# Kernel tuning notes

Measured on AMD Instinct MI355X. Metric: run time of the kernel, lower is better.

## Reference

```python
import jax, jax.numpy as jnp
import numpy as np
from jax import lax

K = 3
STRIDE = 1
PAD = 1
DIL = 1


def _rrsvm(x, s):
    # x: [B, C, H, W], s: [C, K, K]
    B, C, H, W = x.shape
    # im2col: [B, C*K*K, Ho, Wo], channel-major patch ordering -> reshape (C, K*K)
    patches = lax.conv_general_dilated_patches(
        x, (K, K), (STRIDE, STRIDE), [(PAD, PAD), (PAD, PAD)],
        rhs_dilation=(DIL, DIL))
    Ho, Wo = patches.shape[2], patches.shape[3]
    p = patches.reshape(B, C, K * K, Ho, Wo)
    # descending sort of each window's values (rank pooling order)
    order = jnp.argsort(-p, axis=2)                      # [B, C, K*K, Ho, Wo]
    sorted_p = jnp.take_along_axis(p, order, axis=2)
    # learned per-rank weights, per channel
    out = jnp.einsum('bckhw,ck->bchw', sorted_p, s.reshape(C, K * K))
    indices = jnp.transpose(order, (0, 1, 3, 4, 2))      # [B, C, Ho, Wo, K*K]
    return out, indices


def setup_inputs() -> dict:
    key = jax.random.key(0)
    k1, k2 = jax.random.split(key)
    B, C, H, W = 16, 128, 56, 56
    x = jax.random.normal(k1, (B, C, H, W), dtype=jnp.float32)
    # module inits s to 1/(C*K*K); use random positive weights for a non-degenerate test
    s = jax.random.uniform(k2, (C, K, K), dtype=jnp.float32) / (K * K)
    return {"x": x, "s": s}


def reference(x, s):
    return _rrsvm(x, s)
```

## Files before the change

### kernel.cpp

```cpp
#include <hip/hip_runtime.h>


#define B_ 16
#define C_ 128
#define H_ 56
#define W_ 56
#define NPIX (B_*C_*H_*W_)
#define BLK 256
#define PXB (BLK * 2)

typedef float v4f __attribute__((ext_vector_type(4)));

__device__ __forceinline__ void sort9(float v[9], float id[9]) {
    #pragma unroll
    for (int rnd = 0; rnd < 9; ++rnd) {
        #pragma unroll
        for (int i = (rnd & 1); i + 1 < 9; i += 2) {
            float vi = v[i], vj = v[i + 1];
            float ii = id[i], ij = id[i + 1];
            bool sw = vj > vi;
            v[i]      = sw ? vj : vi;  v[i + 1]  = sw ? vi : vj;
            id[i]     = sw ? ij : ii;  id[i + 1] = sw ? ii : ij;
        }
    }
}

__global__ __launch_bounds__(BLK) void rrsvm_kernel(
    const float* __restrict__ x, const float* __restrict__ s,
    float* __restrict__ out, float* __restrict__ idxout)
{
    __shared__ float lds[PXB * 9];

    const int tid = threadIdx.x;
    const int pix = (blockIdx.x * BLK + tid) * 2;
    const int w0  = pix % W_;
    const int t   = pix / W_;
    const int h   = t % H_;
    const int bc  = t / H_;
    const int c   = bc & (C_ - 1);

    const float* sp = s + c * 9;
    float sw9[9];
    #pragma unroll
    for (int r = 0; r < 9; ++r) sw9[r] = sp[r];

    const float* img = x + (size_t)bc * (H_ * W_);
    const int r0 = (h > 0)       ? h - 1  : 0;
    const int r2 = (h < H_ - 1)  ? h + 1  : H_ - 1;
    const int c0 = (w0 > 0)      ? w0 - 1 : 0;
    const int c3 = (w0 < W_ - 2) ? w0 + 2 : W_ - 1;
    const float* p0 = img + r0 * W_;
    const float* p1 = img + h  * W_;
    const float* p2 = img + r2 * W_;

    float tap[3][4];
    tap[0][0] = p0[c0]; tap[0][1] = p0[w0]; tap[0][2] = p0[w0 + 1]; tap[0][3] = p0[c3];
    tap[1][0] = p1[c0]; tap[1][1] = p1[w0]; tap[1][2] = p1[w0 + 1]; tap[1][3] = p1[c3];
    tap[2][0] = p2[c0]; tap[2][1] = p2[w0]; tap[2][2] = p2[w0 + 1]; tap[2][3] = p2[c3];

    const bool rv0 = (h > 0), rv2 = (h < H_ - 1);
    const bool cvL = (w0 > 0), cvR = (w0 < W_ - 2);
    tap[0][0] = (rv0 && cvL) ? tap[0][0] : 0.0f;
    tap[0][1] = rv0          ? tap[0][1] : 0.0f;
    tap[0][2] = rv0          ? tap[0][2] : 0.0f;
    tap[0][3] = (rv0 && cvR) ? tap[0][3] : 0.0f;
    tap[1][0] = cvL          ? tap[1][0] : 0.0f;
    tap[1][3] = cvR          ? tap[1][3] : 0.0f;
    tap[2][0] = (rv2 && cvL) ? tap[2][0] : 0.0f;
    tap[2][1] = rv2          ? tap[2][1] : 0.0f;
    tap[2][2] = rv2          ? tap[2][2] : 0.0f;
    tap[2][3] = (rv2 && cvR) ? tap[2][3] : 0.0f;

    float* lbase = lds + tid * 18;
    float2 o;

    {
        float v[9]  = { tap[0][0], tap[0][1], tap[0][2],
                        tap[1][0], tap[1][1], tap[1][2],
                        tap[2][0], tap[2][1], tap[2][2] };
        float id[9] = { 0, 1, 2, 3, 4, 5, 6, 7, 8 };
        sort9(v, id);
        float acc = 0.0f;
        #pragma unroll
        for (int r = 0; r < 9; ++r) acc = fmaf(v[r], sw9[r], acc);
        o.x = acc;
        #pragma unroll
        for (int r = 0; r < 9; ++r) lbase[r] = id[r];
    }
    {
        float v[9]  = { tap[0][1], tap[0][2], tap[0][3],
                        tap[1][1], tap[1][2], tap[1][3],
                        tap[2][1], tap[2][2], tap[2][3] };
        float id[9] = { 0, 1, 2, 3, 4, 5, 6, 7, 8 };
        sort9(v, id);
        float acc = 0.0f;
        #pragma unroll
        for (int r = 0; r < 9; ++r) acc = fmaf(v[r], sw9[r], acc);
        o.y = acc;
        #pragma unroll
        for (int r = 0; r < 9; ++r) lbase[9 + r] = id[r];
    }

    *(float2*)(out + pix) = o;

    __syncthreads();

    v4f* dst = (v4f*)(idxout + (size_t)blockIdx.x * (PXB * 9));
    const v4f* src = (const v4f*)lds;
    __builtin_nontemporal_store(src[tid],        dst + tid);
    __builtin_nontemporal_store(src[tid + 256],  dst + tid + 256);
    __builtin_nontemporal_store(src[tid + 512],  dst + tid + 512);
    __builtin_nontemporal_store(src[tid + 768],  dst + tid + 768);
    if (tid < 128)
        __builtin_nontemporal_store(src[tid + 1024], dst + tid + 1024);
}

extern "C" void kernel_launch(void* const* d_in, const int* in_sizes, int n_in,
                              void* d_out, int out_size, void* d_ws, size_t ws_size,
                              hipStream_t stream) {
    const float* x = (const float*)d_in[0];
    const float* s = (const float*)d_in[1];
    float* out    = (float*)d_out;
    float* idxout = out + NPIX;

    const int nblocks = NPIX / PXB;
    rrsvm_kernel<<<nblocks, BLK, 0, stream>>>(x, s, out, idxout);
}
```

Before: 279.3 us.

## Process four pixels per thread and store indices directly without LDS staging

Each thread now handles four horizontally adjacent pixels, reusing a 3x6 tap window loaded with vector reads. The LDS transpose and block barrier for the index output are removed, and each thread writes its 36 indices with nine 16-byte stores. This cuts redundant loads and the barrier. In exchange it uses more registers, has strided per-instruction stores, and drops the nontemporal hints.

```diff
diff --git a/kernel.cpp b/kernel.cpp
--- a/kernel.cpp
+++ b/kernel.cpp
@@ -7,7 +7,7 @@
 #define W_ 56
 #define NPIX (B_*C_*H_*W_)
 #define BLK 256
-#define PXB (BLK * 2)
+#define PXT 4
 
 typedef float v4f __attribute__((ext_vector_type(4)));
 
@@ -29,15 +29,13 @@
     const float* __restrict__ x, const float* __restrict__ s,
     float* __restrict__ out, float* __restrict__ idxout)
 {
-    __shared__ float lds[PXB * 9];
-
-    const int tid = threadIdx.x;
-    const int pix = (blockIdx.x * BLK + tid) * 2;
-    const int w0  = pix % W_;
-    const int t   = pix / W_;
-    const int h   = t % H_;
-    const int bc  = t / H_;
-    const int c   = bc & (C_ - 1);
+    const int gtid = blockIdx.x * BLK + threadIdx.x;
+    const int pix0 = gtid * PXT;
+    const int w0   = pix0 % W_;
+    const int t    = pix0 / W_;
+    const int h    = t % H_;
+    const int bc   = t / H_;
+    const int c    = bc & (C_ - 1);
 
     const float* sp = s + c * 9;
     float sw9[9];
@@ -45,74 +43,65 @@
     for (int r = 0; r < 9; ++r) sw9[r] = sp[r];
 
     const float* img = x + (size_t)bc * (H_ * W_);
-    const int r0 = (h > 0)       ? h - 1  : 0;
-    const int r2 = (h < H_ - 1)  ? h + 1  : H_ - 1;
-    const int c0 = (w0 > 0)      ? w0 - 1 : 0;
-    const int c3 = (w0 < W_ - 2) ? w0 + 2 : W_ - 1;
+    const int r0 = (h > 0)      ? h - 1 : 0;
+    const int r2 = (h < H_ - 1) ? h + 1 : H_ - 1;
+    const int cl = (w0 > 0)        ? w0 - 1 : 0;
+    const int cr = (w0 < W_ - PXT) ? w0 + 4 : W_ - 1;
     const float* p0 = img + r0 * W_;
     const float* p1 = img + h  * W_;
     const float* p2 = img + r2 * W_;
 
-    float tap[3][4];
-    tap[0][0] = p0[c0]; tap[0][1] = p0[w0]; tap[0][2] = p0[w0 + 1]; tap[0][3] = p0[c3];
-    tap[1][0] = p1[c0]; tap[1][1] = p1[w0]; tap[1][2] = p1[w0 + 1]; tap[1][3] = p1[c3];
-    tap[2][0] = p2[c0]; tap[2][1] = p2[w0]; tap[2][2] = p2[w0 + 1]; tap[2][3] = p2[c3];
+    float T[3][6];
+    {
+        v4f m0 = *(const v4f*)(p0 + w0);
+        v4f m1 = *(const v4f*)(p1 + w0);
+        v4f m2 = *(const v4f*)(p2 + w0);
+        T[0][0] = p0[cl]; T[0][1] = m0.x; T[0][2] = m0.y; T[0][3] = m0.z; T[0][4] = m0.w; T[0][5] = p0[cr];
+        T[1][0] = p1[cl]; T[1][1] = m1.x; T[1][2] = m1.y; T[1][3] = m1.z; T[1][4] = m1.w; T[1][5] = p1[cr];
+        T[2][0] = p2[cl]; T[2][1] = m2.x; T[2][2] = m2.y; T[2][3] = m2.z; T[2][4] = m2.w; T[2][5] = p2[cr];
+    }
 
     const bool rv0 = (h > 0), rv2 = (h < H_ - 1);
-    const bool cvL = (w0 > 0), cvR = (w0 < W_ - 2);
-    tap[0][0] = (rv0 && cvL) ? tap[0][0] : 0.0f;
-    tap[0][1] = rv0          ? tap[0][1] : 0.0f;
-    tap[0][2] = rv0          ? tap[0][2] : 0.0f;
-    tap[0][3] = (rv0 && cvR) ? tap[0][3] : 0.0f;
-    tap[1][0] = cvL          ? tap[1][0] : 0.0f;
-    tap[1][3] = cvR          ? tap[1][3] : 0.0f;
-    tap[2][0] = (rv2 && cvL) ? tap[2][0] : 0.0f;
-    tap[2][1] = rv2          ? tap[2][1] : 0.0f;
-    tap[2][2] = rv2          ? tap[2][2] : 0.0f;
-    tap[2][3] = (rv2 && cvR) ? tap[2][3] : 0.0f;
+    const bool cvL = (w0 > 0), cvR = (w0 < W_ - PXT);
+    #pragma unroll
+    for (int j = 0; j < 6; ++j) {
+        T[0][j] = rv0 ? T[0][j] : 0.0f;
+        T[2][j] = rv2 ? T[2][j] : 0.0f;
+    }
+    T[0][0] = cvL ? T[0][0] : 0.0f;
+    T[1][0] = cvL ? T[1][0] : 0.0f;
+    T[2][0] = cvL ? T[2][0] : 0.0f;
+    T[0][5] = cvR ? T[0][5] : 0.0f;
+    T[1][5] = cvR ? T[1][5] : 0.0f;
+    T[2][5] = cvR ? T[2][5] : 0.0f;
 
-    float* lbase = lds + tid * 18;
-    float2 o;
+    float idxf[36];
+    v4f o;
+    float oacc[4];
 
-    {
-        float v[9]  = { tap[0][0], tap[0][1], tap[0][2],
-                        tap[1][0], tap[1][1], tap[1][2],
-                        tap[2][0], tap[2][1], tap[2][2] };
+    #pragma unroll
+    for (int j = 0; j < PXT; ++j) {
+        float v[9]  = { T[0][j], T[0][j+1], T[0][j+2],
+                        T[1][j], T[1][j+1], T[1][j+2],
+                        T[2][j], T[2][j+1], T[2][j+2] };
         float id[9] = { 0, 1, 2, 3, 4, 5, 6, 7, 8 };
         sort9(v, id);
         float acc = 0.0f;
         #pragma unroll
         for (int r = 0; r < 9; ++r) acc = fmaf(v[r], sw9[r], acc);
-        o.x = acc;
+        oacc[j] = acc;
         #pragma unroll
-        for (int r = 0; r < 9; ++r) lbase[r] = id[r];
+        for (int r = 0; r < 9; ++r) idxf[j * 9 + r] = id[r];
     }
-    {
-        float v[9]  = { tap[0][1], tap[0][2], tap[0][3],
-                        tap[1][1], tap[1][2], tap[1][3],
-                        tap[2][1], tap[2][2], tap[2][3] };
-        float id[9] = { 0, 1, 2, 3, 4, 5, 6, 7, 8 };
-        sort9(v, id);
-        float acc = 0.0f;
-        #pragma unroll
-        for (int r = 0; r < 9; ++r) acc = fmaf(v[r], sw9[r], acc);
-        o.y = acc;
-        #pragma unroll
-        for (int r = 0; r < 9; ++r) lbase[9 + r] = id[r];
-    }
+    o.x = oacc[0]; o.y = oacc[1]; o.z = oacc[2]; o.w = oacc[3];
 
-    *(float2*)(out + pix) = o;
+    *(v4f*)(out + pix0) = o;
 
-    __syncthreads();
-
-    v4f* dst = (v4f*)(idxout + (size_t)blockIdx.x * (PXB * 9));
-    const v4f* src = (const v4f*)lds;
-    __builtin_nontemporal_store(src[tid],        dst + tid);
-    __builtin_nontemporal_store(src[tid + 256],  dst + tid + 256);
-    __builtin_nontemporal_store(src[tid + 512],  dst + tid + 512);
-    __builtin_nontemporal_store(src[tid + 768],  dst + tid + 768);
-    if (tid < 128)
-        __builtin_nontemporal_store(src[tid + 1024], dst + tid + 1024);
+    v4f* dst = (v4f*)(idxout + (size_t)gtid * 36);
+    const v4f* srcv = (const v4f*)idxf;
+    #pragma unroll
+    for (int k = 0; k < 9; ++k)
+        dst[k] = srcv[k];
 }
 
 extern "C" void kernel_launch(void* const* d_in, const int* in_sizes, int n_in,
@@ -123,6 +112,6 @@
     float* out    = (float*)d_out;
     float* idxout = out + NPIX;
 
-    const int nblocks = NPIX / PXB;
+    const int nblocks = NPIX / (BLK * PXT);
     rrsvm_kernel<<<nblocks, BLK, 0, stream>>>(x, s, out, idxout);
 }
```

Result: slower. 325.2 us (+16.4%).
